# Kernel optimization log

Measured on AMD Instinct MI355X. Metric: run time of the kernel, lower is better.

## Reference

```python
import jax, jax.numpy as jnp
import numpy as np

B, S, E = 8, 2048, 1024


def setup_inputs() -> dict:
    key = jax.random.key(0)
    ks = jax.random.split(key, 8)
    scale = 1.0 / np.sqrt(E)
    x = jax.random.normal(ks[0], (B, S, E), dtype=jnp.float32)
    Wq = jax.random.uniform(ks[1], (E, E), jnp.float32, -scale, scale)
    bq = jax.random.uniform(ks[2], (E,), jnp.float32, -scale, scale)
    Wk = jax.random.uniform(ks[3], (E, E), jnp.float32, -scale, scale)
    bk = jax.random.uniform(ks[4], (E,), jnp.float32, -scale, scale)
    Wv = jax.random.uniform(ks[5], (E, E), jnp.float32, -scale, scale)
    bv = jax.random.uniform(ks[6], (E,), jnp.float32, -scale, scale)
    # key-padding mask: True = fill position (broadcasts over query dim)
    mask = jax.random.randint(ks[7], (B, 1, S), 0, 2) > 0
    return {"x": x, "Wq": Wq, "bq": bq, "Wk": Wk, "bk": bk, "Wv": Wv, "bv": bv, "mask": mask}


def reference(x, Wq, bq, Wk, bk, Wv, bv, mask):
    # torch Linear: y = x @ W.T + b
    q = jnp.einsum('bse,fe->bsf', x, Wq) + bq
    k = jnp.einsum('bse,fe->bsf', x, Wk) + bk
    v = jnp.einsum('bse,fe->bsf', x, Wv) + bv
    inv_sqrt_d = 1.0 / jnp.sqrt(jnp.asarray(E, x.dtype))
    A = jnp.einsum('bqe,bke->bqk', q, k) * inv_sqrt_d  # (B, S, S)
    # non-standard masked_fill: fills with 1e-9 (NOT -inf), pre-softmax
    A = jnp.where(mask, jnp.asarray(1e-9, A.dtype), A)
    A = jax.nn.softmax(A, axis=-1)
    out = jnp.einsum('bqk,bke->bqe', A, v)
    # dropout is identity at inference
    return out
```

## Files before the change

kernel.cpp:

```cpp
#include <hip/hip_runtime.h>
#include <hip/hip_bf16.h>

#define B_ 8
#define S_ 2048
#define E_ 1024

using f32x4 = __attribute__((ext_vector_type(4))) float;
using s16x8 = __attribute__((ext_vector_type(8))) short;
using u16x8 = __attribute__((ext_vector_type(8))) unsigned short;

typedef __attribute__((address_space(1))) unsigned int glb_u32;
typedef __attribute__((address_space(3))) unsigned int lds_u32;

#define FENCE() __builtin_amdgcn_sched_barrier(0)

static __device__ __forceinline__ unsigned short f2bf(float f) {
    union { float f; unsigned int u; } v; v.f = f;
    unsigned int u = v.u;
    u += 0x7FFFu + ((u >> 16) & 1u);
    return (unsigned short)(u >> 16);
}
static __device__ __forceinline__ float bf2f(unsigned short h) {
    union { unsigned int u; float f; } v; v.u = ((unsigned int)h) << 16;
    return v.f;
}

__global__ __launch_bounds__(256) void mask_canon_kernel(
    const unsigned char* __restrict__ src, unsigned char* __restrict__ dst, int n)
{
    __shared__ int flags;
    if (threadIdx.x == 0) flags = 0;
    __syncthreads();
    int f = 0;
    for (int j = threadIdx.x; j < n; j += 256) {
        unsigned char b = src[j];
        if (b) {
            int p = j & 3;
            if (p == 1) f |= 1;
            if (p >= 2) f |= 2;
        }
    }
    if (f) atomicOr(&flags, f);
    __syncthreads();
    const int fl = flags;
    for (int i = threadIdx.x; i < n; i += 256) {
        unsigned char v;
        if (fl & 1)      v = (unsigned char)(src[i] != 0);
        else if (fl & 2) v = (unsigned char)(((const float*)(const void*)src)[i] != 0.0f);
        else             v = (unsigned char)(((const int*)(const void*)src)[i] != 0);
        dst[i] = v;
    }
}

__global__ __launch_bounds__(256) void cvt_all_kernel(
    const float* __restrict__ x,  unsigned short* __restrict__ xb,
    const float* __restrict__ w0, unsigned short* __restrict__ d0,
    const float* __restrict__ w1, unsigned short* __restrict__ d1,
    const float* __restrict__ w2, unsigned short* __restrict__ d2,
    int nx8, int nw8)
{
    const int total = nx8 + 3 * nw8;
    const int stride = gridDim.x * 256;
    for (int i = blockIdx.x * 256 + threadIdx.x; i < total; i += stride) {
        const float* s; unsigned short* d; int k;
        if (i < nx8)                { s = x;  d = xb; k = i; }
        else if (i < nx8 + nw8)     { s = w0; d = d0; k = i - nx8; }
        else if (i < nx8 + 2 * nw8) { s = w1; d = d1; k = i - nx8 - nw8; }
        else                        { s = w2; d = d2; k = i - nx8 - 2 * nw8; }
        float4 a = *(const float4*)(s + (size_t)k * 8);
        float4 b = *(const float4*)(s + (size_t)k * 8 + 4);
        u16x8 o;
        o[0]=f2bf(a.x); o[1]=f2bf(a.y); o[2]=f2bf(a.z); o[3]=f2bf(a.w);
        o[4]=f2bf(b.x); o[5]=f2bf(b.y); o[6]=f2bf(b.z); o[7]=f2bf(b.w);
        *(u16x8*)(d + (size_t)k * 8) = o;
    }
}

__global__ __launch_bounds__(256) void invrs_kernel(
    const float* __restrict__ psum, float* __restrict__ invrs, int n)
{
    int i = blockIdx.x * 256 + threadIdx.x;
    if (i < n) {
        const float* p = psum + (size_t)i * 8;
        float s = ((p[0] + p[1]) + (p[2] + p[3])) + ((p[4] + p[5]) + (p[6] + p[7]));
        invrs[i] = 1.0f / s;
    }
}

template<int EPI>
__global__ __launch_bounds__(512, 2) void gemm256(
    const unsigned short* __restrict__ A, const unsigned short* __restrict__ B,
    void* __restrict__ Cout,
    long long sAz, long long sBz, long long sCz,
    int lda, int ldb, int ldc, int K,
    const unsigned char* __restrict__ mask, int maskStride, float scale,
    const float* __restrict__ bias,
    const unsigned short* __restrict__ B2, const float* __restrict__ bias2,
    void* __restrict__ Cout2, float* __restrict__ aux)
{
    __shared__ unsigned short lds[65536];
    const int tid = threadIdx.x;
    const int lane = tid & 63, w = tid >> 6;
    const int wr = w >> 2, wc = w & 3;
    const int fr = lane & 15, ch = lane >> 4;

    const int gx = gridDim.x, gy = gridDim.y;
    const int nwg = gx * gy * gridDim.z;
    int bid = blockIdx.x + gx * (blockIdx.y + gy * blockIdx.z);
    bid = (bid & 7) * (nwg >> 3) + (bid >> 3);
    const int bx = bid % gx; int tmp = bid / gx;
    const int by = tmp % gy; const int bz = tmp / gy;

    const unsigned short* Ab = A + (size_t)bz * sAz;
    const unsigned short* Bb = B + (size_t)bz * sBz;
    const float* biasv = bias;
    void* Coutv = Cout;
    const int m0 = by * 256;
    int n0 = bx * 256;
    if constexpr (EPI == 4) {
        if (n0 >= 1024) { Bb = B2; biasv = bias2; Coutv = Cout2; n0 -= 1024; }
    }

    const int rdlane = fr * 32 + ((ch * 8) ^ ((fr & 8) ? 16 : 0));
    const int local = (lane * 16) ^ (lane & 32);
    const int rloc = local >> 6;
    const int cloc = (local >> 4) & 3;

    f32x4 acc[8][4] = {};
    const int NT = K >> 5;

    auto STAGE = [&](const unsigned short* __restrict__ src, int ld, int base,
                     int ts, int half, int matoff, unsigned bufo) {
        const int rowb = half * 128 + w * 16;
        const unsigned short* g = src + (size_t)(base + rowb + rloc) * ld
                                      + (ts * 32 + cloc * 8);
        __builtin_amdgcn_global_load_lds((const glb_u32*)g,
            (lds_u32*)&lds[bufo + matoff + rowb * 32], 16, 0, 0);
    };
    auto STAGE_TILE = [&](int ts, unsigned bufo) {
        STAGE(Ab, lda, m0, ts, 0, 0, bufo);
        STAGE(Ab, lda, m0, ts, 1, 0, bufo);
        STAGE(Bb, ldb, n0, ts, 0, 8192, bufo);
        STAGE(Bb, ldb, n0, ts, 1, 8192, bufo);
    };

    STAGE_TILE(0, 0);
    STAGE_TILE((1 < NT) ? 1 : 0, 16384);
    asm volatile("s_waitcnt vmcnt(4)" ::: "memory");
    __builtin_amdgcn_s_barrier();

    unsigned cur = 0, nxt = 16384, stg = 32768;
    for (int t = 0; t < NT; ++t) {
        const int tp2 = (t + 2 < NT) ? t + 2 : NT - 1;

        s16x8 af[8], bfv[4];
        #pragma unroll
        for (int i = 0; i < 4; ++i)
            af[i] = *(const s16x8*)&lds[cur + (wr * 128 + i * 16) * 32 + rdlane];
        #pragma unroll
        for (int j = 0; j < 2; ++j)
            bfv[j] = *(const s16x8*)&lds[cur + 8192 + (wc * 64 + j * 16) * 32 + rdlane];
        FENCE();
        #pragma unroll
        for (int i = 4; i < 8; ++i)
            af[i] = *(const s16x8*)&lds[cur + (wr * 128 + i * 16) * 32 + rdlane];
        #pragma unroll
        for (int j = 2; j < 4; ++j)
            bfv[j] = *(const s16x8*)&lds[cur + 8192 + (wc * 64 + j * 16) * 32 + rdlane];
        STAGE_TILE(tp2, stg);
        FENCE();
        asm volatile("s_waitcnt lgkmcnt(6)" ::: "memory");
        FENCE();
        __builtin_amdgcn_s_setprio(1);
        #pragma unroll
        for (int i = 0; i < 4; ++i)
            #pragma unroll
            for (int j = 0; j < 2; ++j)
                acc[i][j] = __builtin_amdgcn_mfma_f32_16x16x32_bf16(af[i], bfv[j], acc[i][j], 0, 0, 0);
        __builtin_amdgcn_s_setprio(0);
        FENCE();
        asm volatile("s_waitcnt lgkmcnt(0)" ::: "memory");
        FENCE();
        __builtin_amdgcn_s_setprio(1);
        #pragma unroll
        for (int i = 0; i < 4; ++i)
            #pragma unroll
            for (int j = 2; j < 4; ++j)
                acc[i][j] = __builtin_amdgcn_mfma_f32_16x16x32_bf16(af[i], bfv[j], acc[i][j], 0, 0, 0);
        #pragma unroll
        for (int i = 4; i < 8; ++i)
            #pragma unroll
            for (int j = 0; j < 4; ++j)
                acc[i][j] = __builtin_amdgcn_mfma_f32_16x16x32_bf16(af[i], bfv[j], acc[i][j], 0, 0, 0);
        __builtin_amdgcn_s_setprio(0);
        FENCE();
        asm volatile("s_waitcnt vmcnt(4)" ::: "memory");
        FENCE();
        __builtin_amdgcn_s_barrier();
        const unsigned tmpb = cur; cur = nxt; nxt = stg; stg = tmpb;
    }

    asm volatile("s_waitcnt vmcnt(0) lgkmcnt(0)" ::: "memory");
    __builtin_amdgcn_s_barrier();

    if constexpr (EPI == 1) {
        float* Cb = (float*)Coutv + (size_t)bz * sCz;
        const float* invrs = aux;
        float* lf = (float*)lds;
        #pragma unroll
        for (int p = 0; p < 2; ++p) {
            if (p == 1) __syncthreads();
            #pragma unroll
            for (int j = 0; j < 4; ++j) {
                const int lcol = wc * 64 + j * 16 + fr;
                #pragma unroll
                for (int i = 0; i < 4; ++i)
                    #pragma unroll
                    for (int r = 0; r < 4; ++r) {
                        const int lrow = wr * 64 + i * 16 + ch * 4 + r;
                        lf[lrow * 256 + lcol] = acc[4 * p + i][j][r];
                    }
            }
            __syncthreads();
            #pragma unroll
            for (int s = 0; s < 16; ++s) {
                const int lrow = s * 8 + (tid >> 6);
                const int colf = (tid & 63) * 4;
                float4 v = *(const float4*)&lf[lrow * 256 + colf];
                const int mrow = m0 + ((lrow >= 64) ? 128 : 0) + p * 64 + (lrow & 63);
                const float irs = invrs[(size_t)bz * S_ + mrow];
                v.x *= irs; v.y *= irs; v.z *= irs; v.w *= irs;
                *(float4*)&Cb[(size_t)mrow * ldc + n0 + colf] = v;
            }
        }
    } else {
        unsigned short* Cb = (unsigned short*)Coutv + (size_t)bz * sCz;
        const unsigned char* mb = (EPI == 0) ? mask + (size_t)bz * maskStride : nullptr;
        #pragma unroll
        for (int j = 0; j < 4; ++j) {
            const int lcol = wc * 64 + j * 16 + fr;
            bool msk = false; float bn = 0.f;
            if constexpr (EPI == 0) msk = mb[n0 + lcol] != 0;
            if constexpr (EPI == 2 || EPI == 4) bn = biasv[n0 + lcol];
            #pragma unroll
            for (int i = 0; i < 8; ++i) {
                #pragma unroll
                for (int r = 0; r < 4; ++r) {
                    const int lrow = wr * 128 + i * 16 + ch * 4 + r;
                    float val;
                    if constexpr (EPI == 0)      val = msk ? 1.0f : __expf(acc[i][j][r] * scale);
                    else if constexpr (EPI == 2 || EPI == 4) val = acc[i][j][r] + bn;
                    else                         val = acc[i][j][r] + biasv[m0 + lrow];
                    lds[lrow * 256 + lcol] = f2bf(val);
                }
            }
        }
        __syncthreads();
        if constexpr (EPI == 0) {
            const int row = tid >> 1, half = tid & 1;
            float s = 0.f;
            #pragma unroll
            for (int c = 0; c < 16; ++c) {
                const int cc = (c + row) & 15;
                u16x8 v8 = *(const u16x8*)&lds[row * 256 + half * 128 + cc * 8];
                #pragma unroll
                for (int e = 0; e < 8; ++e) s += bf2f(v8[e]);
            }
            s += __shfl_xor(s, 1, 64);
            if (half == 0)
                aux[((size_t)bz * S_ + m0 + row) * 8 + bx] = s;
        }
        #pragma unroll
        for (int s = 0; s < 16; ++s) {
            const int lrow = s * 16 + (tid >> 5);
            const int colu = (tid & 31) * 8;
            u16x8 v = *(const u16x8*)&lds[lrow * 256 + colu];
            *(u16x8*)&Cb[(size_t)(m0 + lrow) * ldc + n0 + colu] = v;
        }
    }
}

extern "C" void kernel_launch(void* const* d_in, const int* in_sizes, int n_in,
                              void* d_out, int out_size, void* d_ws, size_t ws_size,
                              hipStream_t stream)
{
    const float* x  = (const float*)d_in[0];
    const float* Wq = (const float*)d_in[1];
    const float* bq = (const float*)d_in[2];
    const float* Wk = (const float*)d_in[3];
    const float* bk = (const float*)d_in[4];
    const float* Wv = (const float*)d_in[5];
    const float* bv = (const float*)d_in[6];
    const unsigned char* mraw = (const unsigned char*)d_in[7];

    const int BS = B_ * S_;
    unsigned short* Qb = (unsigned short*)d_ws;
    unsigned short* Kb = Qb + (size_t)BS * E_;
    unsigned short* VT = Kb + (size_t)BS * E_;
    unsigned short* Sc = VT + (size_t)BS * E_;
    unsigned short* xb = Sc;
    unsigned short* Wqb = Sc + (size_t)BS * E_;
    unsigned short* Wkb = Wqb + (size_t)E_ * E_;
    unsigned short* Wvb = Wkb + (size_t)E_ * E_;
    unsigned char* mcanon = (unsigned char*)(Sc + (size_t)B_ * S_ * S_);
    float* psum = (float*)(mcanon + 65536);
    float* invr = psum + (size_t)BS * 8;

    mask_canon_kernel<<<1, 256, 0, stream>>>(mraw, mcanon, BS);

    cvt_all_kernel<<<2048, 256, 0, stream>>>(
        x, xb, Wq, Wqb, Wk, Wkb, Wv, Wvb, BS * E_ / 8, E_ * E_ / 8);

    gemm256<4><<<dim3(2048 / 256, BS / 256), 512, 0, stream>>>(
        xb, Wqb, (void*)Qb, 0, 0, 0, E_, E_, E_, E_, nullptr, 0, 1.0f, bq,
        Wkb, bk, (void*)Kb, nullptr);
    gemm256<3><<<dim3(BS / 256, E_ / 256), 512, 0, stream>>>(
        Wvb, xb, (void*)VT, 0, 0, 0, E_, E_, BS, E_, nullptr, 0, 1.0f, bv,
        nullptr, nullptr, nullptr, nullptr);

    gemm256<0><<<dim3(S_ / 256, S_ / 256, B_), 512, 0, stream>>>(
        Qb, Kb, (void*)Sc,
        (long long)S_ * E_, (long long)S_ * E_, (long long)S_ * S_,
        E_, E_, S_, E_, mcanon, S_, 0.03125f, nullptr,
        nullptr, nullptr, nullptr, psum);

    invrs_kernel<<<BS / 256, 256, 0, stream>>>(psum, invr, BS);

    gemm256<1><<<dim3(E_ / 256, S_ / 256, B_), 512, 0, stream>>>(
        Sc, VT, d_out,
        (long long)S_ * S_, (long long)S_, (long long)S_ * E_,
        S_, BS, E_, S_, nullptr, 0, 1.0f, nullptr,
        nullptr, nullptr, nullptr, invr);
}
```

Measured before the change: 317.2 us.

## Use 1024-thread GEMM workgroups and fold row-sum reciprocal into PV epilogue

Doubles the GEMM workgroup from 8 to 16 waves over the same 256x256 tile, so each wave holds a 64x64 accumulator instead of 128x64. Staging loads are split so half the waves load A and half load B. This halves per-wave register pressure and adds more waves for latency hiding. Separately, the invrs kernel is removed and the PV epilogue sums the eight partial softmax denominators and takes the reciprocal inline, saving one launch. The risks are more barrier contention across 16 waves, less MFMA work per LDS read, and the launch bound (1024,4) may not be achievable with 128KB of LDS per block.

```diff
diff --git a/kernel.cpp b/kernel.cpp
--- a/kernel.cpp
+++ b/kernel.cpp
@@ -76,19 +76,8 @@
     }
 }
 
-__global__ __launch_bounds__(256) void invrs_kernel(
-    const float* __restrict__ psum, float* __restrict__ invrs, int n)
-{
-    int i = blockIdx.x * 256 + threadIdx.x;
-    if (i < n) {
-        const float* p = psum + (size_t)i * 8;
-        float s = ((p[0] + p[1]) + (p[2] + p[3])) + ((p[4] + p[5]) + (p[6] + p[7]));
-        invrs[i] = 1.0f / s;
-    }
-}
-
 template<int EPI>
-__global__ __launch_bounds__(512, 2) void gemm256(
+__global__ __launch_bounds__(1024, 4) void gemm256(
     const unsigned short* __restrict__ A, const unsigned short* __restrict__ B,
     void* __restrict__ Cout,
     long long sAz, long long sBz, long long sCz,
@@ -126,54 +115,56 @@
     const int rloc = local >> 6;
     const int cloc = (local >> 4) & 3;
 
-    f32x4 acc[8][4] = {};
+    f32x4 acc[4][4] = {};
     const int NT = K >> 5;
 
-    auto STAGE = [&](const unsigned short* __restrict__ src, int ld, int base,
-                     int ts, int half, int matoff, unsigned bufo) {
-        const int rowb = half * 128 + w * 16;
-        const unsigned short* g = src + (size_t)(base + rowb + rloc) * ld
-                                      + (ts * 32 + cloc * 8);
-        __builtin_amdgcn_global_load_lds((const glb_u32*)g,
-            (lds_u32*)&lds[bufo + matoff + rowb * 32], 16, 0, 0);
-    };
+    const unsigned short* ssrc = (w < 8) ? Ab : Bb;
+    const int sld   = (w < 8) ? lda : ldb;
+    const int sbase = (w < 8) ? m0 : n0;
+    const int smat  = (w < 8) ? 0 : 8192;
+    const int srow0 = (w & 7) * 32;
+
     auto STAGE_TILE = [&](int ts, unsigned bufo) {
-        STAGE(Ab, lda, m0, ts, 0, 0, bufo);
-        STAGE(Ab, lda, m0, ts, 1, 0, bufo);
-        STAGE(Bb, ldb, n0, ts, 0, 8192, bufo);
-        STAGE(Bb, ldb, n0, ts, 1, 8192, bufo);
+        #pragma unroll
+        for (int half = 0; half < 2; ++half) {
+            const int rowb = srow0 + half * 16;
+            const unsigned short* g = ssrc + (size_t)(sbase + rowb + rloc) * sld
+                                          + (ts * 32 + cloc * 8);
+            __builtin_amdgcn_global_load_lds((const glb_u32*)g,
+                (lds_u32*)&lds[bufo + smat + rowb * 32], 16, 0, 0);
+        }
     };
 
     STAGE_TILE(0, 0);
     STAGE_TILE((1 < NT) ? 1 : 0, 16384);
-    asm volatile("s_waitcnt vmcnt(4)" ::: "memory");
+    asm volatile("s_waitcnt vmcnt(2)" ::: "memory");
     __builtin_amdgcn_s_barrier();
 
     unsigned cur = 0, nxt = 16384, stg = 32768;
     for (int t = 0; t < NT; ++t) {
         const int tp2 = (t + 2 < NT) ? t + 2 : NT - 1;
 
-        s16x8 af[8], bfv[4];
-        #pragma unroll
-        for (int i = 0; i < 4; ++i)
-            af[i] = *(const s16x8*)&lds[cur + (wr * 128 + i * 16) * 32 + rdlane];
+        s16x8 af[4], bfv[4];
+        #pragma unroll
+        for (int i = 0; i < 2; ++i)
+            af[i] = *(const s16x8*)&lds[cur + (wr * 64 + i * 16) * 32 + rdlane];
         #pragma unroll
         for (int j = 0; j < 2; ++j)
             bfv[j] = *(const s16x8*)&lds[cur + 8192 + (wc * 64 + j * 16) * 32 + rdlane];
         FENCE();
         #pragma unroll
-        for (int i = 4; i < 8; ++i)
-            af[i] = *(const s16x8*)&lds[cur + (wr * 128 + i * 16) * 32 + rdlane];
+        for (int i = 2; i < 4; ++i)
+            af[i] = *(const s16x8*)&lds[cur + (wr * 64 + i * 16) * 32 + rdlane];
         #pragma unroll
         for (int j = 2; j < 4; ++j)
             bfv[j] = *(const s16x8*)&lds[cur + 8192 + (wc * 64 + j * 16) * 32 + rdlane];
         STAGE_TILE(tp2, stg);
         FENCE();
-        asm volatile("s_waitcnt lgkmcnt(6)" ::: "memory");
+        asm volatile("s_waitcnt lgkmcnt(4)" ::: "memory");
         FENCE();
         __builtin_amdgcn_s_setprio(1);
         #pragma unroll
-        for (int i = 0; i < 4; ++i)
+        for (int i = 0; i < 2; ++i)
             #pragma unroll
             for (int j = 0; j < 2; ++j)
                 acc[i][j] = __builtin_amdgcn_mfma_f32_16x16x32_bf16(af[i], bfv[j], acc[i][j], 0, 0, 0);
@@ -183,18 +174,18 @@
         FENCE();
         __builtin_amdgcn_s_setprio(1);
         #pragma unroll
-        for (int i = 0; i < 4; ++i)
+        for (int i = 0; i < 2; ++i)
             #pragma unroll
             for (int j = 2; j < 4; ++j)
                 acc[i][j] = __builtin_amdgcn_mfma_f32_16x16x32_bf16(af[i], bfv[j], acc[i][j], 0, 0, 0);
         #pragma unroll
-        for (int i = 4; i < 8; ++i)
+        for (int i = 2; i < 4; ++i)
             #pragma unroll
             for (int j = 0; j < 4; ++j)
                 acc[i][j] = __builtin_amdgcn_mfma_f32_16x16x32_bf16(af[i], bfv[j], acc[i][j], 0, 0, 0);
         __builtin_amdgcn_s_setprio(0);
         FENCE();
-        asm volatile("s_waitcnt vmcnt(4)" ::: "memory");
+        asm volatile("s_waitcnt vmcnt(2)" ::: "memory");
         FENCE();
         __builtin_amdgcn_s_barrier();
         const unsigned tmpb = cur; cur = nxt; nxt = stg; stg = tmpb;
@@ -205,30 +196,34 @@
 
     if constexpr (EPI == 1) {
         float* Cb = (float*)Coutv + (size_t)bz * sCz;
-        const float* invrs = aux;
         float* lf = (float*)lds;
         #pragma unroll
         for (int p = 0; p < 2; ++p) {
             if (p == 1) __syncthreads();
-            #pragma unroll
-            for (int j = 0; j < 4; ++j) {
-                const int lcol = wc * 64 + j * 16 + fr;
+            if ((wr >> 1) == p) {
                 #pragma unroll
-                for (int i = 0; i < 4; ++i)
+                for (int j = 0; j < 4; ++j) {
+                    const int lcol = wc * 64 + j * 16 + fr;
                     #pragma unroll
-                    for (int r = 0; r < 4; ++r) {
-                        const int lrow = wr * 64 + i * 16 + ch * 4 + r;
-                        lf[lrow * 256 + lcol] = acc[4 * p + i][j][r];
-                    }
+                    for (int i = 0; i < 4; ++i)
+                        #pragma unroll
+                        for (int r = 0; r < 4; ++r) {
+                            const int lrow = (wr & 1) * 64 + i * 16 + ch * 4 + r;
+                            lf[lrow * 256 + lcol] = acc[i][j][r];
+                        }
+                }
             }
             __syncthreads();
             #pragma unroll
-            for (int s = 0; s < 16; ++s) {
-                const int lrow = s * 8 + (tid >> 6);
+            for (int s = 0; s < 8; ++s) {
+                const int lrow = s * 16 + (tid >> 6);
                 const int colf = (tid & 63) * 4;
                 float4 v = *(const float4*)&lf[lrow * 256 + colf];
-                const int mrow = m0 + ((lrow >= 64) ? 128 : 0) + p * 64 + (lrow & 63);
-                const float irs = invrs[(size_t)bz * S_ + mrow];
+                const int mrow = m0 + p * 128 + lrow;
+                const float* pp = aux + ((size_t)bz * S_ + mrow) * 8;
+                const float ssum = ((pp[0] + pp[1]) + (pp[2] + pp[3]))
+                                 + ((pp[4] + pp[5]) + (pp[6] + pp[7]));
+                const float irs = 1.0f / ssum;
                 v.x *= irs; v.y *= irs; v.z *= irs; v.w *= irs;
                 *(float4*)&Cb[(size_t)mrow * ldc + n0 + colf] = v;
             }
@@ -241,15 +236,15 @@
             const int lcol = wc * 64 + j * 16 + fr;
             bool msk = false; float bn = 0.f;
             if constexpr (EPI == 0) msk = mb[n0 + lcol] != 0;
-            if constexpr (EPI == 2 || EPI == 4) bn = biasv[n0 + lcol];
-            #pragma unroll
-            for (int i = 0; i < 8; ++i) {
+            if constexpr (EPI == 4) bn = biasv[n0 + lcol];
+            #pragma unroll
+            for (int i = 0; i < 4; ++i) {
                 #pragma unroll
                 for (int r = 0; r < 4; ++r) {
-                    const int lrow = wr * 128 + i * 16 + ch * 4 + r;
+                    const int lrow = wr * 64 + i * 16 + ch * 4 + r;
                     float val;
                     if constexpr (EPI == 0)      val = msk ? 1.0f : __expf(acc[i][j][r] * scale);
-                    else if constexpr (EPI == 2 || EPI == 4) val = acc[i][j][r] + bn;
+                    else if constexpr (EPI == 4) val = acc[i][j][r] + bn;
                     else                         val = acc[i][j][r] + biasv[m0 + lrow];
                     lds[lrow * 256 + lcol] = f2bf(val);
                 }
@@ -257,22 +252,23 @@
         }
         __syncthreads();
         if constexpr (EPI == 0) {
-            const int row = tid >> 1, half = tid & 1;
+            const int row = tid >> 2, q = tid & 3;
             float s = 0.f;
             #pragma unroll
-            for (int c = 0; c < 16; ++c) {
-                const int cc = (c + row) & 15;
-                u16x8 v8 = *(const u16x8*)&lds[row * 256 + half * 128 + cc * 8];
+            for (int c = 0; c < 8; ++c) {
+                const int cc = (c + row) & 7;
+                u16x8 v8 = *(const u16x8*)&lds[row * 256 + q * 64 + cc * 8];
                 #pragma unroll
                 for (int e = 0; e < 8; ++e) s += bf2f(v8[e]);
             }
             s += __shfl_xor(s, 1, 64);
-            if (half == 0)
+            s += __shfl_xor(s, 2, 64);
+            if (q == 0)
                 aux[((size_t)bz * S_ + m0 + row) * 8 + bx] = s;
         }
         #pragma unroll
-        for (int s = 0; s < 16; ++s) {
-            const int lrow = s * 16 + (tid >> 5);
+        for (int s = 0; s < 8; ++s) {
+            const int lrow = s * 32 + (tid >> 5);
             const int colu = (tid & 31) * 8;
             u16x8 v = *(const u16x8*)&lds[lrow * 256 + colu];
             *(u16x8*)&Cb[(size_t)(m0 + lrow) * ldc + n0 + colu] = v;
@@ -304,31 +300,28 @@
     unsigned short* Wvb = Wkb + (size_t)E_ * E_;
     unsigned char* mcanon = (unsigned char*)(Sc + (size_t)B_ * S_ * S_);
     float* psum = (float*)(mcanon + 65536);
-    float* invr = psum + (size_t)BS * 8;
 
     mask_canon_kernel<<<1, 256, 0, stream>>>(mraw, mcanon, BS);
 
     cvt_all_kernel<<<2048, 256, 0, stream>>>(
         x, xb, Wq, Wqb, Wk, Wkb, Wv, Wvb, BS * E_ / 8, E_ * E_ / 8);
 
-    gemm256<4><<<dim3(2048 / 256, BS / 256), 512, 0, stream>>>(
+    gemm256<4><<<dim3(2048 / 256, BS / 256), 1024, 0, stream>>>(
         xb, Wqb, (void*)Qb, 0, 0, 0, E_, E_, E_, E_, nullptr, 0, 1.0f, bq,
         Wkb, bk, (void*)Kb, nullptr);
-    gemm256<3><<<dim3(BS / 256, E_ / 256), 512, 0, stream>>>(
+    gemm256<3><<<dim3(BS / 256, E_ / 256), 1024, 0, stream>>>(
         Wvb, xb, (void*)VT, 0, 0, 0, E_, E_, BS, E_, nullptr, 0, 1.0f, bv,
         nullptr, nullptr, nullptr, nullptr);
 
-    gemm256<0><<<dim3(S_ / 256, S_ / 256, B_), 512, 0, stream>>>(
+    gemm256<0><<<dim3(S_ / 256, S_ / 256, B_), 1024, 0, stream>>>(
         Qb, Kb, (void*)Sc,
         (long long)S_ * E_, (long long)S_ * E_, (long long)S_ * S_,
         E_, E_, S_, E_, mcanon, S_, 0.03125f, nullptr,
         nullptr, nullptr, nullptr, psum);
 
-    invrs_kernel<<<BS / 256, 256, 0, stream>>>(psum, invr, BS);
-
-    gemm256<1><<<dim3(E_ / 256, S_ / 256, B_), 512, 0, stream>>>(
+    gemm256<1><<<dim3(E_ / 256, S_ / 256, B_), 1024, 0, stream>>>(
         Sc, VT, d_out,
         (long long)S_ * S_, (long long)S_, (long long)S_ * E_,
         S_, BS, E_, S_, nullptr, 0, 1.0f, nullptr,
-        nullptr, nullptr, nullptr, invr);
-}
+        nullptr, nullptr, nullptr, psum);
+}
```

After: 316.0 us. No clear change (-0.4%).
